# Optimization experiments

Measured on AMD Instinct MI355X. Metric: run time of the kernel, lower is better.

Reference implementation:

```python
import jax, jax.numpy as jnp
import numpy as np

B, L, D = 256, 512, 512

def setup_inputs() -> dict:
    key = jax.random.key(0)
    k1, k2, k3, k4, k5 = jax.random.split(key, 5)
    scale = 1.0 / np.sqrt(D)  # keep logits in a sane range
    return {
        "text_features": jax.random.normal(k1, (B, L, D), dtype=jnp.float32),
        "image_features": jax.random.normal(k2, (B, D), dtype=jnp.float32),
        "W_ML": jax.random.normal(k3, (D, D), dtype=jnp.float32) * scale,
        "W_MV": jax.random.normal(k4, (D, D), dtype=jnp.float32) * scale,
        "tau": jnp.ones((1,), dtype=jnp.float32),
        "padding_mask": jax.random.randint(k5, (B, L), 0, 2).astype(bool),
    }

def reference(text_features, image_features, W_ML, W_MV, tau, padding_mask):
    b, l, _ = text_features.shape
    tau_c = jnp.clip(tau, 0.001)  # [1]
    valid = ~padding_mask  # [B,L] True where token is real
    # Linear(bias=False): y = x @ W.T
    text_proj = jnp.einsum('bld,ed->ble', text_features, W_ML)   # [B,L,D]
    image_proj = jnp.einsum('bd,ed->be', image_features, W_MV)   # [B,D]
    neg_inf = jnp.float32(-jnp.inf)
    # positive scores: own image vs own text tokens
    s_iji = jnp.einsum('bd,bld->bl', image_proj, text_proj) / tau_c  # [B,L]
    # all-images-vs-text denominator: s_kji[i,l,k] = <text[i,l], image[k]>
    s_kji = jnp.einsum('ild,kd->ilk', text_proj, image_proj) / tau_c  # [B,L,B]
    mask_kj = valid.T[None, :, :]  # [1,L,B] -> valid[k,l] per (i,l,k)
    s_kji = jnp.where(mask_kj, s_kji, neg_inf)
    denom_log = jax.nn.logsumexp(s_kji, axis=2)  # [B,L]
    # cross-batch text negatives: s_iok[i,k,l] = <image[i], text[k,l]>
    s_iok = jnp.einsum('id,kld->ikl', image_proj, text_proj) / tau_c  # [B,B,L]
    mask_ko = valid[None, :, :]  # [1,B,L]
    mask_neq = ~jnp.eye(b, dtype=bool)[:, :, None]  # exclude k == i
    s_iok_f = jnp.where(mask_ko & mask_neq, s_iok, neg_inf).reshape(b, -1)
    cross_log = jax.nn.logsumexp(s_iok_f, axis=1)  # [B]
    neg_log = jnp.logaddexp(s_iji, cross_log[:, None])  # [B,L]
    denom_log = jnp.where(valid, denom_log, 0.0)
    neg_log = jnp.where(valid, neg_log, 0.0)
    f1 = denom_log - s_iji
    f2 = neg_log - s_iji
    loss_mat = 0.5 * (f1 + f2)
    n_valid = jnp.sum(valid)
    loss = jnp.sum(jnp.where(valid, loss_mat, 0.0)) / n_valid
    return loss
```

## Files before the change

### kernel.cpp

```cpp
#include <hip/hip_runtime.h>
#include <math.h>


#define B_ 256
#define L_ 512
#define D_ 512
#define ROWS (B_ * L_)
#define NT (ROWS / 64)
#define NEG_INF (-INFINITY)

typedef __attribute__((ext_vector_type(8))) short s8_t;
typedef __attribute__((ext_vector_type(4))) float f4_t;
typedef __attribute__((ext_vector_type(2))) float f2_t;
typedef __attribute__((ext_vector_type(4))) unsigned short us4_t;

__device__ inline unsigned short f2bf(float x) {
    unsigned int u = __float_as_uint(x);
    u += 0x7FFFu + ((u >> 16) & 1u);
    return (unsigned short)(u >> 16);
}

__global__ __launch_bounds__(256) void ip_kernel(const float* __restrict__ img,
                                                 const float* __restrict__ Wmv,
                                                 float* __restrict__ ip) {
    int kt = blockIdx.x >> 3, et = blockIdx.x & 7;
    __shared__ float Ast[32][36];
    __shared__ float Bst[32][72];
    int tid = threadIdx.x;
    int ty = tid >> 4;
    int tx = tid & 15;
    float acc[2][4] = {};
    int sr = tid >> 3, sc = (tid & 7) * 4;
    for (int d0 = 0; d0 < D_; d0 += 32) {
        f4_t a = *(const f4_t*)(img + (size_t)(kt * 32 + sr) * D_ + d0 + sc);
        f4_t b0 = *(const f4_t*)(Wmv + (size_t)(et * 64 + sr) * D_ + d0 + sc);
        f4_t b1 = *(const f4_t*)(Wmv + (size_t)(et * 64 + sr + 32) * D_ + d0 + sc);
        __syncthreads();
#pragma unroll
        for (int m = 0; m < 4; m++) {
            Ast[sc + m][sr] = a[m];
            Bst[sc + m][sr] = b0[m];
            Bst[sc + m][sr + 32] = b1[m];
        }
        __syncthreads();
#pragma unroll 4
        for (int d = 0; d < 32; d++) {
            f2_t a2 = *(const f2_t*)&Ast[d][ty * 2];
            f4_t b4 = *(const f4_t*)&Bst[d][tx * 4];
#pragma unroll
            for (int i = 0; i < 2; i++)
#pragma unroll
                for (int j = 0; j < 4; j++) acc[i][j] = fmaf(a2[i], b4[j], acc[i][j]);
        }
    }
#pragma unroll
    for (int i = 0; i < 2; i++) {
        f4_t o; o[0] = acc[i][0]; o[1] = acc[i][1]; o[2] = acc[i][2]; o[3] = acc[i][3];
        *(f4_t*)(ip + (size_t)(kt * 32 + ty * 2 + i) * D_ + et * 64 + tx * 4) = o;
    }
}

__global__ __launch_bounds__(256) void c_kernel(const float* __restrict__ ip,
                                                const float* __restrict__ Wml,
                                                const float* __restrict__ tau,
                                                unsigned short* __restrict__ Cb) {
    int kt = blockIdx.x >> 3, dt = blockIdx.x & 7;
    __shared__ float Ast[32][36];
    __shared__ float Bst[32][72];
    int tid = threadIdx.x;
    int ty = tid >> 4;
    int tx = tid & 15;
    float acc[2][4] = {};
    int sr = tid >> 3, sc = (tid & 7) * 4;
    int br = tid >> 4, bc = (tid & 15) * 4;
    for (int e0 = 0; e0 < D_; e0 += 32) {
        f4_t a = *(const f4_t*)(ip + (size_t)(kt * 32 + sr) * D_ + e0 + sc);
        f4_t b0 = *(const f4_t*)(Wml + (size_t)(e0 + br) * D_ + dt * 64 + bc);
        f4_t b1 = *(const f4_t*)(Wml + (size_t)(e0 + br + 16) * D_ + dt * 64 + bc);
        __syncthreads();
#pragma unroll
        for (int m = 0; m < 4; m++) Ast[sc + m][sr] = a[m];
        *(f4_t*)&Bst[br][bc] = b0;
        *(f4_t*)&Bst[br + 16][bc] = b1;
        __syncthreads();
#pragma unroll 4
        for (int e = 0; e < 32; e++) {
            f2_t a2 = *(const f2_t*)&Ast[e][ty * 2];
            f4_t b4 = *(const f4_t*)&Bst[e][tx * 4];
#pragma unroll
            for (int i = 0; i < 2; i++)
#pragma unroll
                for (int j = 0; j < 4; j++) acc[i][j] = fmaf(a2[i], b4[j], acc[i][j]);
        }
    }
    float it = 1.0f / fmaxf(tau[0], 0.001f);
#pragma unroll
    for (int i = 0; i < 2; i++) {
        us4_t o;
#pragma unroll
        for (int j = 0; j < 4; j++) o[j] = f2bf(acc[i][j] * it);
        *(us4_t*)(Cb + (size_t)(kt * 32 + ty * 2 + i) * D_ + dt * 64 + tx * 4) = o;
    }
}

__global__ __launch_bounds__(256) void mask_kernel(const int* __restrict__ pad,
                                                   unsigned long long* __restrict__ mbits) {
    int l = blockIdx.x;
    int w = threadIdx.x >> 6;
    int j = threadIdx.x & 63;
    unsigned long long bal = __ballot(pad[(w * 64 + j) * L_ + l] == 0);
    if (j == 0) mbits[l * 4 + w] = bal;
}

struct StageRegs { f4_t av0, av1; s8_t bv0, bv1, bv2, bv3; };

__device__ __attribute__((always_inline)) inline void g_load(
    const float* aptr, const unsigned short* bptr, int koff, StageRegs& r) {
    r.av0 = *(const f4_t*)(aptr + koff);
    r.av1 = *(const f4_t*)(aptr + koff + 4);
    r.bv0 = *(const s8_t*)(bptr + koff);
    r.bv1 = *(const s8_t*)(bptr + (size_t)64 * D_ + koff);
    r.bv2 = *(const s8_t*)(bptr + (size_t)128 * D_ + koff);
    r.bv3 = *(const s8_t*)(bptr + (size_t)192 * D_ + koff);
}

__device__ __attribute__((always_inline)) inline void lds_store(
    unsigned short* a_s, unsigned short* b_s, int arow, int akq, int bn, int bkq,
    const StageRegs& r) {
    s8_t a8;
    a8[0] = (short)f2bf(r.av0[0]); a8[1] = (short)f2bf(r.av0[1]);
    a8[2] = (short)f2bf(r.av0[2]); a8[3] = (short)f2bf(r.av0[3]);
    a8[4] = (short)f2bf(r.av1[0]); a8[5] = (short)f2bf(r.av1[1]);
    a8[6] = (short)f2bf(r.av1[2]); a8[7] = (short)f2bf(r.av1[3]);
    *(s8_t*)(a_s + arow * 40 + akq * 8) = a8;
    *(s8_t*)(b_s + (bn + 0) * 40 + bkq * 8)   = r.bv0;
    *(s8_t*)(b_s + (bn + 64) * 40 + bkq * 8)  = r.bv1;
    *(s8_t*)(b_s + (bn + 128) * 40 + bkq * 8) = r.bv2;
    *(s8_t*)(b_s + (bn + 192) * 40 + bkq * 8) = r.bv3;
}

__device__ __attribute__((always_inline)) inline void do_mfma(
    const unsigned short* a_s, const unsigned short* b_s, int mm, int qd, int wave,
    f4_t acc[4][4]) {
    s8_t af[4], bf[4];
#pragma unroll
    for (int mt = 0; mt < 4; mt++)
        af[mt] = *(const s8_t*)(a_s + (mt * 16 + mm) * 40 + qd * 8);
#pragma unroll
    for (int nt = 0; nt < 4; nt++)
        bf[nt] = *(const s8_t*)(b_s + (wave * 64 + nt * 16 + mm) * 40 + qd * 8);
#pragma unroll
    for (int mt = 0; mt < 4; mt++)
#pragma unroll
        for (int nt = 0; nt < 4; nt++)
            acc[mt][nt] = __builtin_amdgcn_mfma_f32_16x16x32_bf16(
                af[mt], bf[nt], acc[mt][nt], 0, 0, 0);
}

__global__ __launch_bounds__(256) void gemm_mfma_kernel(
    const float* __restrict__ text, const unsigned short* __restrict__ Cb,
    const unsigned long long* __restrict__ mbits,
    float* __restrict__ denom, float* __restrict__ siji,
    float* __restrict__ crossM, float* __restrict__ crossS) {
    __shared__ __align__(16) float lds[12800];
    unsigned short* A0 = (unsigned short*)lds;
    unsigned short* Bb0 = A0 + 2560;
    unsigned short* A1 = A0 + 12800;
    unsigned short* Bb1 = A1 + 2560;
    float* Sh  = lds;
    float* pm  = lds + 8224;
    float* ps  = lds + 8352;
    float* rvadj = lds + 8480;

    const int tile = blockIdx.x;
    const int row0 = tile * 64;
    const int bIdx = row0 >> 9;
    const int l0 = row0 & 511;
    const int tid = threadIdx.x;
    const int wave = tid >> 6;
    const int lane = tid & 63;
    const int qd = lane >> 4;
    const int mm = lane & 15;

    f4_t acc[4][4];
#pragma unroll
    for (int mt = 0; mt < 4; mt++)
#pragma unroll
        for (int nt = 0; nt < 4; nt++)
#pragma unroll
            for (int r = 0; r < 4; r++) acc[mt][nt][r] = 0.f;

    const int arow = tid >> 2, akq = tid & 3;
    const float* aptr = text + (size_t)(row0 + arow) * D_ + akq * 8;
    const int bkq = tid & 3, bn = tid >> 2;
    const unsigned short* bptr = Cb + (size_t)bn * D_ + bkq * 8;

    StageRegs rg;
    g_load(aptr, bptr, 0, rg);
    lds_store(A0, Bb0, arow, akq, bn, bkq, rg);
#pragma unroll 1
    for (int k0 = 0; k0 < 16; k0 += 2) {
        g_load(aptr, bptr, (k0 + 1) * 32, rg);
        __syncthreads();
        do_mfma(A0, Bb0, mm, qd, wave, acc);
        lds_store(A1, Bb1, arow, akq, bn, bkq, rg);
        bool more = (k0 + 2) < 16;
        if (more) g_load(aptr, bptr, (k0 + 2) * 32, rg);
        __syncthreads();
        do_mfma(A1, Bb1, mm, qd, wave, acc);
        if (more) lds_store(A0, Bb0, arow, akq, bn, bkq, rg);
    }

    float cm = NEG_INF, cs = 0.f;
    const int mw = bIdx >> 6, mb = bIdx & 63;

#pragma unroll
    for (int h = 0; h < 2; h++) {
        __syncthreads();
#pragma unroll
        for (int mt2 = 0; mt2 < 2; mt2++) {
            int mt = h * 2 + mt2;
            int rl = mt2 * 16 + qd * 4;
#pragma unroll
            for (int nt = 0; nt < 4; nt++) {
                int col = wave * 64 + nt * 16 + mm;
#pragma unroll
                for (int r = 0; r < 4; r++)
                    Sh[(rl + r) * 257 + col] = acc[mt][nt][r];
            }
        }
        if (tid < 32) {
            int l = l0 + h * 32 + tid;
            rvadj[tid] = ((mbits[l * 4 + mw] >> mb) & 1ULL) ? 0.f : NEG_INF;
        }
        __syncthreads();

        {
            float m2 = NEG_INF;
#pragma unroll 8
            for (int r = 0; r < 32; r++)
                m2 = fmaxf(m2, Sh[r * 257 + tid] + rvadj[r]);
            if (m2 > NEG_INF) {
                float s2 = 0.f;
#pragma unroll 8
                for (int r = 0; r < 32; r++)
                    s2 += __expf(Sh[r * 257 + tid] + rvadj[r] - m2);
                float M = fmaxf(cm, m2);
                cs = cs * __expf(cm - M) + s2 * __expf(m2 - M);
                cm = M;
            }
        }
        if (tid < 128) {
            int row = tid & 31, grp = tid >> 5;
            int l = l0 + h * 32 + row;
            unsigned long long bits = mbits[l * 4 + grp];
            const float* Srow = Sh + row * 257 + grp * 64;
            float m = NEG_INF;
#pragma unroll 8
            for (int c = 0; c < 64; c++) {
                float adj = ((bits >> c) & 1ULL) ? 0.f : NEG_INF;
                m = fmaxf(m, Srow[c] + adj);
            }
            float s = 0.f;
            if (m > NEG_INF) {
#pragma unroll 8
                for (int c = 0; c < 64; c++) {
                    float adj = ((bits >> c) & 1ULL) ? 0.f : NEG_INF;
                    s += __expf(Srow[c] + adj - m);
                }
            }
            pm[grp * 32 + row] = m;
            ps[grp * 32 + row] = s;
        }
        __syncthreads();
        if (tid < 32) {
            float m0 = pm[tid], m1 = pm[32 + tid], m2 = pm[64 + tid], m3 = pm[96 + tid];
            float M = fmaxf(fmaxf(m0, m1), fmaxf(m2, m3));
            float dl;
            if (M == NEG_INF) dl = NEG_INF;
            else {
                float s = ps[tid] * __expf(m0 - M) + ps[32 + tid] * __expf(m1 - M) +
                          ps[64 + tid] * __expf(m2 - M) + ps[96 + tid] * __expf(m3 - M);
                dl = M + __logf(s);
            }
            int gr = row0 + h * 32 + tid;
            denom[gr] = dl;
            siji[gr] = Sh[tid * 257 + bIdx];
        }
    }
    if (tid == bIdx) { cm = NEG_INF; cs = 0.f; }
    crossM[(size_t)tid * NT + tile] = cm;
    crossS[(size_t)tid * NT + tile] = cs;
}

__global__ __launch_bounds__(256) void cross_combine_kernel(const float* __restrict__ crossM,
                                                            const float* __restrict__ crossS,
                                                            float* __restrict__ crossLog) {
    int i = blockIdx.x;
    int tid = threadIdx.x;
    float m = NEG_INF, s = 0.f;
    for (int e = 0; e < NT / 256; e++) {
        int t = e * 256 + tid;
        float m2 = crossM[(size_t)i * NT + t];
        float s2 = crossS[(size_t)i * NT + t];
        if (m2 > NEG_INF) {
            if (m == NEG_INF) { m = m2; s = s2; }
            else {
                float M = fmaxf(m, m2);
                s = s * expf(m - M) + s2 * expf(m2 - M);
                m = M;
            }
        }
    }
    __shared__ float sm[256], ss[256];
    sm[tid] = m; ss[tid] = s;
    __syncthreads();
    for (int off = 128; off > 0; off >>= 1) {
        if (tid < off) {
            float m1 = sm[tid], s1 = ss[tid];
            float m2 = sm[tid + off], s2 = ss[tid + off];
            float M = fmaxf(m1, m2);
            float sv;
            if (M == NEG_INF) sv = 0.f;
            else sv = s1 * expf(m1 - M) + s2 * expf(m2 - M);
            sm[tid] = M; ss[tid] = sv;
        }
        __syncthreads();
    }
    if (tid == 0) crossLog[i] = (sm[0] == NEG_INF) ? NEG_INF : sm[0] + logf(ss[0]);
}

__global__ __launch_bounds__(256) void loss_partial_kernel(
    const int* __restrict__ pad, const float* __restrict__ denom,
    const float* __restrict__ siji, const float* __restrict__ crossLog,
    float* __restrict__ psum, float* __restrict__ pcnt) {
    int tid = threadIdx.x;
    int idx = blockIdx.x * 256 + tid;
    float term = 0.f, cnt = 0.f;
    if (pad[idx] == 0) {
        float dl = denom[idx], sv = siji[idx], cl = crossLog[idx >> 9];
        float M = fmaxf(sv, cl);
        float neg = M + log1pf(expf(-fabsf(sv - cl)));
        term = 0.5f * (dl + neg) - sv;
        cnt = 1.f;
    }
    __shared__ float bs[256], bc[256];
    bs[tid] = term; bc[tid] = cnt;
    __syncthreads();
    for (int off = 128; off > 0; off >>= 1) {
        if (tid < off) { bs[tid] += bs[tid + off]; bc[tid] += bc[tid + off]; }
        __syncthreads();
    }
    if (tid == 0) { psum[blockIdx.x] = bs[0]; pcnt[blockIdx.x] = bc[0]; }
}

__global__ __launch_bounds__(256) void final_kernel(const float* __restrict__ psum,
                                                    const float* __restrict__ pcnt,
                                                    float* __restrict__ out) {
    int tid = threadIdx.x;
    __shared__ float bs[256], bc[256];
    bs[tid] = psum[tid] + psum[tid + 256];
    bc[tid] = pcnt[tid] + pcnt[tid + 256];
    __syncthreads();
    for (int off = 128; off > 0; off >>= 1) {
        if (tid < off) { bs[tid] += bs[tid + off]; bc[tid] += bc[tid + off]; }
        __syncthreads();
    }
    if (tid == 0) out[0] = bs[0] / bc[0];
}

extern "C" void kernel_launch(void* const* d_in, const int* in_sizes, int n_in,
                              void* d_out, int out_size, void* d_ws, size_t ws_size,
                              hipStream_t stream) {
    (void)in_sizes; (void)n_in; (void)out_size; (void)ws_size;
    const float* text = (const float*)d_in[0];
    const float* img  = (const float*)d_in[1];
    const float* Wml  = (const float*)d_in[2];
    const float* Wmv  = (const float*)d_in[3];
    const float* tau  = (const float*)d_in[4];
    const int* pad    = (const int*)d_in[5];
    float* out = (float*)d_out;

    float* ws = (float*)d_ws;
    float* ip       = ws;
    unsigned short* Cb = (unsigned short*)(ws + 131072);
    unsigned long long* mbits = (unsigned long long*)(ws + 262144);
    float* denom    = ws + 266240;
    float* siji     = ws + 397312;
    float* crossM   = ws + 528384;
    float* crossS   = ws + 1052672;
    float* crossLog = ws + 1576960;
    float* psum     = ws + 1577216;
    float* pcnt     = ws + 1577728;

    hipLaunchKernelGGL(ip_kernel,   dim3(64),  dim3(256), 0, stream, img, Wmv, ip);
    hipLaunchKernelGGL(c_kernel,    dim3(64),  dim3(256), 0, stream, ip, Wml, tau, Cb);
    hipLaunchKernelGGL(mask_kernel, dim3(L_),  dim3(256), 0, stream, pad, mbits);
    hipLaunchKernelGGL(gemm_mfma_kernel, dim3(NT), dim3(256), 0, stream,
                       text, Cb, mbits, denom, siji, crossM, crossS);
    hipLaunchKernelGGL(cross_combine_kernel, dim3(B_), dim3(256), 0, stream,
                       crossM, crossS, crossLog);
    hipLaunchKernelGGL(loss_partial_kernel, dim3(ROWS / 256), dim3(256), 0, stream,
                       pad, denom, siji, crossLog, psum, pcnt);
    hipLaunchKernelGGL(final_kernel, dim3(1), dim3(256), 0, stream, psum, pcnt, out);
}
```

Baseline: 495.1 us.

## Use 128-row GEMM tiles and read the B operand straight from global memory

Each GEMM block now covers 128 text rows instead of 64, which halves the grid and doubles each wave's accumulator tile to 8x4 MFMA fragments. The B operand (the bf16 combined image projection) is no longer staged through LDS; each wave loads its fragments directly from global/L2 every k-step. Only the A tile is double-buffered in LDS, so there is one barrier per k-step instead of the previous paired stages. The goal is to cut LDS traffic and synchronisation and to reuse B across more rows. In exchange, register pressure rises, which may lower occupancy, and uncoalesced B loads from L2 may stall the MFMAs.

Measured after the change: 565.1 us. 14.1% more time.

```diff
diff --git a/kernel.cpp b/kernel.cpp
--- a/kernel.cpp
+++ b/kernel.cpp
@@ -6,7 +6,7 @@
 #define L_ 512
 #define D_ 512
 #define ROWS (B_ * L_)
-#define NT (ROWS / 64)
+#define NT2 (ROWS / 128)
 #define NEG_INF (-INFINITY)
 
 typedef __attribute__((ext_vector_type(8))) short s8_t;
@@ -112,68 +112,21 @@
     if (j == 0) mbits[l * 4 + w] = bal;
 }
 
-struct StageRegs { f4_t av0, av1; s8_t bv0, bv1, bv2, bv3; };
-
-__device__ __attribute__((always_inline)) inline void g_load(
-    const float* aptr, const unsigned short* bptr, int koff, StageRegs& r) {
-    r.av0 = *(const f4_t*)(aptr + koff);
-    r.av1 = *(const f4_t*)(aptr + koff + 4);
-    r.bv0 = *(const s8_t*)(bptr + koff);
-    r.bv1 = *(const s8_t*)(bptr + (size_t)64 * D_ + koff);
-    r.bv2 = *(const s8_t*)(bptr + (size_t)128 * D_ + koff);
-    r.bv3 = *(const s8_t*)(bptr + (size_t)192 * D_ + koff);
-}
-
-__device__ __attribute__((always_inline)) inline void lds_store(
-    unsigned short* a_s, unsigned short* b_s, int arow, int akq, int bn, int bkq,
-    const StageRegs& r) {
-    s8_t a8;
-    a8[0] = (short)f2bf(r.av0[0]); a8[1] = (short)f2bf(r.av0[1]);
-    a8[2] = (short)f2bf(r.av0[2]); a8[3] = (short)f2bf(r.av0[3]);
-    a8[4] = (short)f2bf(r.av1[0]); a8[5] = (short)f2bf(r.av1[1]);
-    a8[6] = (short)f2bf(r.av1[2]); a8[7] = (short)f2bf(r.av1[3]);
-    *(s8_t*)(a_s + arow * 40 + akq * 8) = a8;
-    *(s8_t*)(b_s + (bn + 0) * 40 + bkq * 8)   = r.bv0;
-    *(s8_t*)(b_s + (bn + 64) * 40 + bkq * 8)  = r.bv1;
-    *(s8_t*)(b_s + (bn + 128) * 40 + bkq * 8) = r.bv2;
-    *(s8_t*)(b_s + (bn + 192) * 40 + bkq * 8) = r.bv3;
-}
-
-__device__ __attribute__((always_inline)) inline void do_mfma(
-    const unsigned short* a_s, const unsigned short* b_s, int mm, int qd, int wave,
-    f4_t acc[4][4]) {
-    s8_t af[4], bf[4];
-#pragma unroll
-    for (int mt = 0; mt < 4; mt++)
-        af[mt] = *(const s8_t*)(a_s + (mt * 16 + mm) * 40 + qd * 8);
-#pragma unroll
-    for (int nt = 0; nt < 4; nt++)
-        bf[nt] = *(const s8_t*)(b_s + (wave * 64 + nt * 16 + mm) * 40 + qd * 8);
-#pragma unroll
-    for (int mt = 0; mt < 4; mt++)
-#pragma unroll
-        for (int nt = 0; nt < 4; nt++)
-            acc[mt][nt] = __builtin_amdgcn_mfma_f32_16x16x32_bf16(
-                af[mt], bf[nt], acc[mt][nt], 0, 0, 0);
-}
-
 __global__ __launch_bounds__(256) void gemm_mfma_kernel(
     const float* __restrict__ text, const unsigned short* __restrict__ Cb,
     const unsigned long long* __restrict__ mbits,
     float* __restrict__ denom, float* __restrict__ siji,
     float* __restrict__ crossM, float* __restrict__ crossS) {
-    __shared__ __align__(16) float lds[12800];
+    __shared__ __align__(16) float lds[8512];
     unsigned short* A0 = (unsigned short*)lds;
-    unsigned short* Bb0 = A0 + 2560;
-    unsigned short* A1 = A0 + 12800;
-    unsigned short* Bb1 = A1 + 2560;
+    unsigned short* A1 = A0 + 5120;
     float* Sh  = lds;
     float* pm  = lds + 8224;
     float* ps  = lds + 8352;
     float* rvadj = lds + 8480;
 
     const int tile = blockIdx.x;
-    const int row0 = tile * 64;
+    const int row0 = tile * 128;
     const int bIdx = row0 >> 9;
     const int l0 = row0 & 511;
     const int tid = threadIdx.x;
@@ -182,40 +135,72 @@
     const int qd = lane >> 4;
     const int mm = lane & 15;
 
-    f4_t acc[4][4];
-#pragma unroll
-    for (int mt = 0; mt < 4; mt++)
+    f4_t acc[8][4];
+#pragma unroll
+    for (int mt = 0; mt < 8; mt++)
 #pragma unroll
         for (int nt = 0; nt < 4; nt++)
 #pragma unroll
             for (int r = 0; r < 4; r++) acc[mt][nt][r] = 0.f;
 
-    const int arow = tid >> 2, akq = tid & 3;
-    const float* aptr = text + (size_t)(row0 + arow) * D_ + akq * 8;
-    const int bkq = tid & 3, bn = tid >> 2;
-    const unsigned short* bptr = Cb + (size_t)bn * D_ + bkq * 8;
-
-    StageRegs rg;
-    g_load(aptr, bptr, 0, rg);
-    lds_store(A0, Bb0, arow, akq, bn, bkq, rg);
+    const int arow = tid >> 1, akh = (tid & 1) * 16;
+    const float* aptr = text + (size_t)(row0 + arow) * D_ + akh;
+    const unsigned short* bptr = Cb + (size_t)(wave * 64 + mm) * D_ + qd * 8;
+
+    f4_t ar0, ar1, ar2, ar3;
+    ar0 = *(const f4_t*)(aptr);  ar1 = *(const f4_t*)(aptr + 4);
+    ar2 = *(const f4_t*)(aptr + 8); ar3 = *(const f4_t*)(aptr + 12);
+    {
+        s8_t h0, h1;
+        h0[0]=(short)f2bf(ar0[0]); h0[1]=(short)f2bf(ar0[1]); h0[2]=(short)f2bf(ar0[2]); h0[3]=(short)f2bf(ar0[3]);
+        h0[4]=(short)f2bf(ar1[0]); h0[5]=(short)f2bf(ar1[1]); h0[6]=(short)f2bf(ar1[2]); h0[7]=(short)f2bf(ar1[3]);
+        h1[0]=(short)f2bf(ar2[0]); h1[1]=(short)f2bf(ar2[1]); h1[2]=(short)f2bf(ar2[2]); h1[3]=(short)f2bf(ar2[3]);
+        h1[4]=(short)f2bf(ar3[0]); h1[5]=(short)f2bf(ar3[1]); h1[6]=(short)f2bf(ar3[2]); h1[7]=(short)f2bf(ar3[3]);
+        *(s8_t*)(A0 + arow * 40 + akh) = h0;
+        *(s8_t*)(A0 + arow * 40 + akh + 8) = h1;
+    }
+
 #pragma unroll 1
-    for (int k0 = 0; k0 < 16; k0 += 2) {
-        g_load(aptr, bptr, (k0 + 1) * 32, rg);
-        __syncthreads();
-        do_mfma(A0, Bb0, mm, qd, wave, acc);
-        lds_store(A1, Bb1, arow, akq, bn, bkq, rg);
-        bool more = (k0 + 2) < 16;
-        if (more) g_load(aptr, bptr, (k0 + 2) * 32, rg);
-        __syncthreads();
-        do_mfma(A1, Bb1, mm, qd, wave, acc);
-        if (more) lds_store(A0, Bb0, arow, akq, bn, bkq, rg);
+    for (int k0 = 0; k0 < 16; k0++) {
+        unsigned short* cur = (k0 & 1) ? A1 : A0;
+        unsigned short* nxt = (k0 & 1) ? A0 : A1;
+        bool more = k0 < 15;
+        if (more) {
+            const float* ap = aptr + (k0 + 1) * 32;
+            ar0 = *(const f4_t*)(ap);  ar1 = *(const f4_t*)(ap + 4);
+            ar2 = *(const f4_t*)(ap + 8); ar3 = *(const f4_t*)(ap + 12);
+        }
+        s8_t bf[4];
+#pragma unroll
+        for (int nt = 0; nt < 4; nt++)
+            bf[nt] = *(const s8_t*)(bptr + (size_t)nt * 16 * D_ + k0 * 32);
+        __syncthreads();
+        s8_t af[8];
+#pragma unroll
+        for (int mt = 0; mt < 8; mt++)
+            af[mt] = *(const s8_t*)(cur + (mt * 16 + mm) * 40 + qd * 8);
+#pragma unroll
+        for (int mt = 0; mt < 8; mt++)
+#pragma unroll
+            for (int nt = 0; nt < 4; nt++)
+                acc[mt][nt] = __builtin_amdgcn_mfma_f32_16x16x32_bf16(
+                    af[mt], bf[nt], acc[mt][nt], 0, 0, 0);
+        if (more) {
+            s8_t h0, h1;
+            h0[0]=(short)f2bf(ar0[0]); h0[1]=(short)f2bf(ar0[1]); h0[2]=(short)f2bf(ar0[2]); h0[3]=(short)f2bf(ar0[3]);
+            h0[4]=(short)f2bf(ar1[0]); h0[5]=(short)f2bf(ar1[1]); h0[6]=(short)f2bf(ar1[2]); h0[7]=(short)f2bf(ar1[3]);
+            h1[0]=(short)f2bf(ar2[0]); h1[1]=(short)f2bf(ar2[1]); h1[2]=(short)f2bf(ar2[2]); h1[3]=(short)f2bf(ar2[3]);
+            h1[4]=(short)f2bf(ar3[0]); h1[5]=(short)f2bf(ar3[1]); h1[6]=(short)f2bf(ar3[2]); h1[7]=(short)f2bf(ar3[3]);
+            *(s8_t*)(nxt + arow * 40 + akh) = h0;
+            *(s8_t*)(nxt + arow * 40 + akh + 8) = h1;
+        }
     }
 
     float cm = NEG_INF, cs = 0.f;
     const int mw = bIdx >> 6, mb = bIdx & 63;
 
 #pragma unroll
-    for (int h = 0; h < 2; h++) {
+    for (int h = 0; h < 4; h++) {
         __syncthreads();
 #pragma unroll
         for (int mt2 = 0; mt2 < 2; mt2++) {
@@ -289,8 +274,8 @@
         }
     }
     if (tid == bIdx) { cm = NEG_INF; cs = 0.f; }
-    crossM[(size_t)tid * NT + tile] = cm;
-    crossS[(size_t)tid * NT + tile] = cs;
+    crossM[(size_t)tid * NT2 + tile] = cm;
+    crossS[(size_t)tid * NT2 + tile] = cs;
 }
 
 __global__ __launch_bounds__(256) void cross_combine_kernel(const float* __restrict__ crossM,
@@ -299,10 +284,10 @@
     int i = blockIdx.x;
     int tid = threadIdx.x;
     float m = NEG_INF, s = 0.f;
-    for (int e = 0; e < NT / 256; e++) {
+    for (int e = 0; e < NT2 / 256; e++) {
         int t = e * 256 + tid;
-        float m2 = crossM[(size_t)i * NT + t];
-        float s2 = crossS[(size_t)i * NT + t];
+        float m2 = crossM[(size_t)i * NT2 + t];
+        float s2 = crossS[(size_t)i * NT2 + t];
         if (m2 > NEG_INF) {
             if (m == NEG_INF) { m = m2; s = s2; }
             else {
@@ -388,15 +373,15 @@
     float* denom    = ws + 266240;
     float* siji     = ws + 397312;
     float* crossM   = ws + 528384;
-    float* crossS   = ws + 1052672;
-    float* crossLog = ws + 1576960;
-    float* psum     = ws + 1577216;
-    float* pcnt     = ws + 1577728;
+    float* crossS   = ws + 790528;
+    float* crossLog = ws + 1052672;
+    float* psum     = ws + 1052928;
+    float* pcnt     = ws + 1053440;
 
     hipLaunchKernelGGL(ip_kernel,   dim3(64),  dim3(256), 0, stream, img, Wmv, ip);
     hipLaunchKernelGGL(c_kernel,    dim3(64),  dim3(256), 0, stream, ip, Wml, tau, Cb);
     hipLaunchKernelGGL(mask_kernel, dim3(L_),  dim3(256), 0, stream, pad, mbits);
-    hipLaunchKernelGGL(gemm_mfma_kernel, dim3(NT), dim3(256), 0, stream,
+    hipLaunchKernelGGL(gemm_mfma_kernel, dim3(NT2), dim3(256), 0, stream,
                        text, Cb, mbits, denom, siji, crossM, crossS);
     hipLaunchKernelGGL(cross_combine_kernel, dim3(B_), dim3(256), 0, stream,
                        crossM, crossS, crossLog);
```

## Load GEMM tiles directly into LDS with swizzled layout, single-buffered K=64 steps

Applied to the files above, without the earlier changes.

Replaces the register-staged, double-buffered global-to-LDS copy with global_load_lds direct transfers, using an XOR swizzle to avoid bank conflicts. K step grows from 32 to 64 and the fp32 text is kept in LDS and converted to bf16 at fragment-load time. This removes register staging and VGPR pressure, but it drops double buffering, so global loads no longer overlap MFMA work. It also adds two barriers per step and redoes the bf16 conversion per wave.

Result: no change. 502.0 us (+1.4%).

```diff
diff --git a/kernel.cpp b/kernel.cpp
--- a/kernel.cpp
+++ b/kernel.cpp
@@ -18,6 +18,12 @@
     unsigned int u = __float_as_uint(x);
     u += 0x7FFFu + ((u >> 16) & 1u);
     return (unsigned short)(u >> 16);
+}
+
+typedef const __attribute__((address_space(1))) unsigned int as1_uint;
+typedef __attribute__((address_space(3))) unsigned int as3_uint;
+__device__ __attribute__((always_inline)) inline void gl_lds16(const void* g, void* l) {
+    __builtin_amdgcn_global_load_lds((as1_uint*)g, (as3_uint*)l, 16, 0, 0);
 }
 
 __global__ __launch_bounds__(256) void ip_kernel(const float* __restrict__ img,
@@ -112,61 +118,12 @@
     if (j == 0) mbits[l * 4 + w] = bal;
 }
 
-struct StageRegs { f4_t av0, av1; s8_t bv0, bv1, bv2, bv3; };
-
-__device__ __attribute__((always_inline)) inline void g_load(
-    const float* aptr, const unsigned short* bptr, int koff, StageRegs& r) {
-    r.av0 = *(const f4_t*)(aptr + koff);
-    r.av1 = *(const f4_t*)(aptr + koff + 4);
-    r.bv0 = *(const s8_t*)(bptr + koff);
-    r.bv1 = *(const s8_t*)(bptr + (size_t)64 * D_ + koff);
-    r.bv2 = *(const s8_t*)(bptr + (size_t)128 * D_ + koff);
-    r.bv3 = *(const s8_t*)(bptr + (size_t)192 * D_ + koff);
-}
-
-__device__ __attribute__((always_inline)) inline void lds_store(
-    unsigned short* a_s, unsigned short* b_s, int arow, int akq, int bn, int bkq,
-    const StageRegs& r) {
-    s8_t a8;
-    a8[0] = (short)f2bf(r.av0[0]); a8[1] = (short)f2bf(r.av0[1]);
-    a8[2] = (short)f2bf(r.av0[2]); a8[3] = (short)f2bf(r.av0[3]);
-    a8[4] = (short)f2bf(r.av1[0]); a8[5] = (short)f2bf(r.av1[1]);
-    a8[6] = (short)f2bf(r.av1[2]); a8[7] = (short)f2bf(r.av1[3]);
-    *(s8_t*)(a_s + arow * 40 + akq * 8) = a8;
-    *(s8_t*)(b_s + (bn + 0) * 40 + bkq * 8)   = r.bv0;
-    *(s8_t*)(b_s + (bn + 64) * 40 + bkq * 8)  = r.bv1;
-    *(s8_t*)(b_s + (bn + 128) * 40 + bkq * 8) = r.bv2;
-    *(s8_t*)(b_s + (bn + 192) * 40 + bkq * 8) = r.bv3;
-}
-
-__device__ __attribute__((always_inline)) inline void do_mfma(
-    const unsigned short* a_s, const unsigned short* b_s, int mm, int qd, int wave,
-    f4_t acc[4][4]) {
-    s8_t af[4], bf[4];
-#pragma unroll
-    for (int mt = 0; mt < 4; mt++)
-        af[mt] = *(const s8_t*)(a_s + (mt * 16 + mm) * 40 + qd * 8);
-#pragma unroll
-    for (int nt = 0; nt < 4; nt++)
-        bf[nt] = *(const s8_t*)(b_s + (wave * 64 + nt * 16 + mm) * 40 + qd * 8);
-#pragma unroll
-    for (int mt = 0; mt < 4; mt++)
-#pragma unroll
-        for (int nt = 0; nt < 4; nt++)
-            acc[mt][nt] = __builtin_amdgcn_mfma_f32_16x16x32_bf16(
-                af[mt], bf[nt], acc[mt][nt], 0, 0, 0);
-}
-
 __global__ __launch_bounds__(256) void gemm_mfma_kernel(
     const float* __restrict__ text, const unsigned short* __restrict__ Cb,
     const unsigned long long* __restrict__ mbits,
     float* __restrict__ denom, float* __restrict__ siji,
     float* __restrict__ crossM, float* __restrict__ crossS) {
-    __shared__ __align__(16) float lds[12800];
-    unsigned short* A0 = (unsigned short*)lds;
-    unsigned short* Bb0 = A0 + 2560;
-    unsigned short* A1 = A0 + 12800;
-    unsigned short* Bb1 = A1 + 2560;
+    __shared__ __align__(16) float lds[12288];
     float* Sh  = lds;
     float* pm  = lds + 8224;
     float* ps  = lds + 8352;
@@ -190,25 +147,57 @@
 #pragma unroll
             for (int r = 0; r < 4; r++) acc[mt][nt][r] = 0.f;
 
-    const int arow = tid >> 2, akq = tid & 3;
-    const float* aptr = text + (size_t)(row0 + arow) * D_ + akq * 8;
-    const int bkq = tid & 3, bn = tid >> 2;
-    const unsigned short* bptr = Cb + (size_t)bn * D_ + bkq * 8;
-
-    StageRegs rg;
-    g_load(aptr, bptr, 0, rg);
-    lds_store(A0, Bb0, arow, akq, bn, bkq, rg);
+    char* ldsc = (char*)lds;
+
 #pragma unroll 1
-    for (int k0 = 0; k0 < 16; k0 += 2) {
-        g_load(aptr, bptr, (k0 + 1) * 32, rg);
-        __syncthreads();
-        do_mfma(A0, Bb0, mm, qd, wave, acc);
-        lds_store(A1, Bb1, arow, akq, bn, bkq, rg);
-        bool more = (k0 + 2) < 16;
-        if (more) g_load(aptr, bptr, (k0 + 2) * 32, rg);
-        __syncthreads();
-        do_mfma(A1, Bb1, mm, qd, wave, acc);
-        if (more) lds_store(A0, Bb0, arow, akq, bn, bkq, rg);
+    for (int k0 = 0; k0 < D_; k0 += 64) {
+        __syncthreads();
+#pragma unroll
+        for (int i = 0; i < 4; i++) {
+            int c = i * 256 + tid;
+            int row = c >> 4, j = c & 15;
+            int jg = j ^ ((row & 7) << 1);
+            const float* g = text + (size_t)(row0 + row) * D_ + k0 + jg * 4;
+            gl_lds16(g, ldsc + (i * 256 + wave * 64) * 16);
+        }
+#pragma unroll
+        for (int i = 0; i < 8; i++) {
+            int c = i * 256 + tid;
+            int col = c >> 3, j = c & 7;
+            int jg = j ^ (col & 7);
+            const unsigned short* g = Cb + (size_t)col * D_ + k0 + jg * 8;
+            gl_lds16(g, ldsc + 16384 + (i * 256 + wave * 64) * 16);
+        }
+        __syncthreads();
+#pragma unroll
+        for (int s = 0; s < 2; s++) {
+            s8_t af[4], bf[4];
+#pragma unroll
+            for (int mt = 0; mt < 4; mt++) {
+                int row = mt * 16 + mm;
+                int j0 = (s * 8 + qd * 2) ^ ((mm & 7) << 1);
+                const f4_t* ap = (const f4_t*)(ldsc + row * 256 + j0 * 16);
+                f4_t x0 = ap[0], x1 = ap[1];
+                s8_t h;
+                h[0] = (short)f2bf(x0[0]); h[1] = (short)f2bf(x0[1]);
+                h[2] = (short)f2bf(x0[2]); h[3] = (short)f2bf(x0[3]);
+                h[4] = (short)f2bf(x1[0]); h[5] = (short)f2bf(x1[1]);
+                h[6] = (short)f2bf(x1[2]); h[7] = (short)f2bf(x1[3]);
+                af[mt] = h;
+            }
+#pragma unroll
+            for (int nt = 0; nt < 4; nt++) {
+                int col = wave * 64 + nt * 16 + mm;
+                int j = (s * 4 + qd) ^ (mm & 7);
+                bf[nt] = *(const s8_t*)(ldsc + 16384 + col * 128 + j * 16);
+            }
+#pragma unroll
+            for (int mt = 0; mt < 4; mt++)
+#pragma unroll
+                for (int nt = 0; nt < 4; nt++)
+                    acc[mt][nt] = __builtin_amdgcn_mfma_f32_16x16x32_bf16(
+                        af[mt], bf[nt], acc[mt][nt], 0, 0, 0);
+        }
     }
 
     float cm = NEG_INF, cs = 0.f;
```
